# Optimization experiments

Measured on AMD Instinct MI355X. Metric: run time of the kernel, lower is better.

## Reference

```python
import jax, jax.numpy as jnp
import numpy as np

N = 128
BATCH = 4096


def _legs_transition(n):
    # HiPPO-LegS transition matrices (measure='legs' branch of transition())
    q = np.arange(n, dtype=np.float64)
    col, row = np.meshgrid(q, q)
    r = 2 * q + 1
    M = -(np.where(row >= col, r, 0) - np.diag(q))
    T = np.sqrt(np.diag(2 * q + 1))
    A = T @ M @ np.linalg.inv(T)   # lower triangular
    B = np.diag(T)                 # (n,)
    return A.astype(np.float32), B.astype(np.float32)


def setup_inputs() -> dict:
    key = jax.random.key(0)
    k1, k2, k3 = jax.random.split(key, 3)
    A, B_vec = _legs_transition(N)
    u = jax.random.normal(k1, (BATCH, N), dtype=jnp.float32)
    v = jax.random.normal(k2, (BATCH,), dtype=jnp.float32)
    # per-example step sizes, realistic small dt
    delta = 0.001 + 0.01 * jax.random.uniform(k3, (BATCH,), dtype=jnp.float32)
    return {"u": u, "v": v, "delta": delta, "A": jnp.asarray(A), "B_vec": jnp.asarray(B_vec)}


def reference(u, v, delta, A, B_vec):
    """Bilinear (Tustin) update, alpha=0.5:
       x = (I - dt/2 A)^{-1} [ (I + dt/2 A) u + dt B v ]
    Matches ManualAdaptiveTransition.bilinear with tensor delta.
    """
    n = A.shape[0]
    dt2 = 0.5 * delta                                   # (B,)
    # forward_mult: (I + dt/2 A) u  == u + dt/2 * (A u)
    x = u + dt2[:, None] * jnp.einsum('ij,bj->bi', A, u)
    # add dt * B * v
    x = x + (delta * v)[:, None] * B_vec
    # inverse_mult: batched lower-triangular solve (I - dt/2 A) y = x
    mat = jnp.eye(n, dtype=u.dtype) - dt2[:, None, None] * A   # (B, n, n)
    solve = jax.vmap(lambda m, b: jax.scipy.linalg.solve_triangular(m, b, lower=True))
    x = solve(mat, x)
    return x
```

## Files before the change

### kernel.cpp

```cpp
#include <hip/hip_runtime.h>


#define HN 128

__global__ __launch_bounds__(64) void hippo_bilinear_kernel(
    const float* __restrict__ u,
    const float* __restrict__ v,
    const float* __restrict__ delta,
    const float* __restrict__ Bv,
    float* __restrict__ out)
{
    const int b = blockIdx.x * blockDim.x + threadIdx.x;

    const float dlt = delta[b];
    const float dt2 = 0.5f * dlt;
    const float dv  = dlt * v[b];

    const float* ub = u   + (size_t)b * HN;
    float*       yb = out + (size_t)b * HN;

    float P = 0.0f;
    float S = 0.0f;

    #pragma unroll
    for (int i0 = 0; i0 < HN; i0 += 4) {
        const float4 u4 = *(const float4*)(ub + i0);
        const float4 b4 = *(const float4*)(Bv + i0);
        const float uu[4] = {u4.x, u4.y, u4.z, u4.w};
        const float vv[4] = {b4.x, b4.y, b4.z, b4.w};
        float yy[4];

        #pragma unroll
        for (int k = 0; k < 4; ++k) {
            const float vi  = vv[k];
            const float ui  = uu[k];
            const float ip1 = (float)(i0 + k + 1);

            float au = -vi * P - ip1 * ui;
            float x  = fmaf(dt2, au, ui);
            x = fmaf(dv, vi, x);

            const float d = fmaf(dt2, ip1, 1.0f);
            float r = __builtin_amdgcn_rcpf(d);
            r = r * fmaf(-d, r, 2.0f);

            const float w = dt2 * vi;
            const float y = fmaf(-w, S, x) * r;
            yy[k] = y;

            P = fmaf(vi, ui, P);
            S = fmaf(vi, y, S);
        }

        float4 y4;
        y4.x = yy[0]; y4.y = yy[1]; y4.z = yy[2]; y4.w = yy[3];
        *(float4*)(yb + i0) = y4;
    }
}

extern "C" void kernel_launch(void* const* d_in, const int* in_sizes, int n_in,
                              void* d_out, int out_size, void* d_ws, size_t ws_size,
                              hipStream_t stream) {
    const float* u     = (const float*)d_in[0];
    const float* v     = (const float*)d_in[1];
    const float* delta = (const float*)d_in[2];
    const float* Bv    = (const float*)d_in[4];
    float* out = (float*)d_out;

    const int batch = in_sizes[1];
    hippo_bilinear_kernel<<<dim3(batch / 64), dim3(64), 0, stream>>>(
        u, v, delta, Bv, out);
}
```

Measured before the change: 10.52 us.

## Parallelize triangular solve across a wavefront via affine prefix scans

Replaces the one-thread-per-row sequential recurrence with one 64-lane wavefront per batch row, each lane handling two elements. The dot-product prefix P and the solve recurrence S are computed with shuffle-based inclusive scans, the latter as a scan over affine maps. This removes the long serial dependency chain and gives coalesced float2 loads and stores instead of strided per-thread row accesses. In exchange it adds shuffle overhead and changes the floating-point summation order.

```diff
diff --git a/kernel.cpp b/kernel.cpp
--- a/kernel.cpp
+++ b/kernel.cpp
@@ -3,59 +3,83 @@
 
 #define HN 128
 
-__global__ __launch_bounds__(64) void hippo_bilinear_kernel(
+__global__ __launch_bounds__(256) void hippo_bilinear_wave_kernel(
     const float* __restrict__ u,
     const float* __restrict__ v,
     const float* __restrict__ delta,
     const float* __restrict__ Bv,
     float* __restrict__ out)
 {
-    const int b = blockIdx.x * blockDim.x + threadIdx.x;
+    const int lane = threadIdx.x & 63;
+    const int row  = blockIdx.x * (blockDim.x >> 6) + (threadIdx.x >> 6);
 
-    const float dlt = delta[b];
+    const float dlt = delta[row];
     const float dt2 = 0.5f * dlt;
-    const float dv  = dlt * v[b];
+    const float dv  = dlt * v[row];
 
-    const float* ub = u   + (size_t)b * HN;
-    float*       yb = out + (size_t)b * HN;
+    const float2 u2 = ((const float2*)(u + (size_t)row * HN))[lane];
+    const float2 b2 = ((const float2*)Bv)[lane];
 
-    float P = 0.0f;
-    float S = 0.0f;
+    const float u0 = u2.x, u1 = u2.y;
+    const float v0 = b2.x, v1 = b2.y;
+    const float ip1_0 = (float)(2 * lane + 1);
+    const float ip1_1 = (float)(2 * lane + 2);
+
+    const float p0 = v0 * u0;
+    const float p1 = v1 * u1;
+    const float ps = p0 + p1;
+    float run = ps;
+    #pragma unroll
+    for (int d = 1; d < 64; d <<= 1) {
+        const float t = __shfl_up(run, d, 64);
+        if (lane >= d) run += t;
+    }
+    const float Pexcl = run - ps;
+    const float P0 = Pexcl;
+    const float P1 = Pexcl + p0;
+
+    float x0 = fmaf(dt2, fmaf(-ip1_0, u0, -v0 * P0), u0);
+    x0 = fmaf(dv, v0, x0);
+    float x1 = fmaf(dt2, fmaf(-ip1_1, u1, -v1 * P1), u1);
+    x1 = fmaf(dv, v1, x1);
+
+    const float den0 = fmaf(dt2, ip1_0, 1.0f);
+    const float den1 = fmaf(dt2, ip1_1, 1.0f);
+    float r0 = __builtin_amdgcn_rcpf(den0);
+    r0 = r0 * fmaf(-den0, r0, 2.0f);
+    float r1 = __builtin_amdgcn_rcpf(den1);
+    r1 = r1 * fmaf(-den1, r1, 2.0f);
+
+    const float w0 = dt2 * v0;
+    const float w1 = dt2 * v1;
+    const float c0 = v0 * r0;
+    const float c1 = v1 * r1;
+    const float a0 = fmaf(-w0, c0, 1.0f);
+    const float b0 = c0 * x0;
+    const float a1 = fmaf(-w1, c1, 1.0f);
+    const float b1 = c1 * x1;
+
+    float Ai = a1 * a0;
+    float Bi = fmaf(a1, b0, b1);
 
     #pragma unroll
-    for (int i0 = 0; i0 < HN; i0 += 4) {
-        const float4 u4 = *(const float4*)(ub + i0);
-        const float4 b4 = *(const float4*)(Bv + i0);
-        const float uu[4] = {u4.x, u4.y, u4.z, u4.w};
-        const float vv[4] = {b4.x, b4.y, b4.z, b4.w};
-        float yy[4];
+    for (int d = 1; d < 64; d <<= 1) {
+        const float tA = __shfl_up(Ai, d, 64);
+        const float tB = __shfl_up(Bi, d, 64);
+        if (lane >= d) {
+            Bi = fmaf(Ai, tB, Bi);
+            Ai = Ai * tA;
+        }
+    }
+    const float Bprev = __shfl_up(Bi, 1, 64);
+    const float Sin = (lane == 0) ? 0.0f : Bprev;
 
-        #pragma unroll
-        for (int k = 0; k < 4; ++k) {
-            const float vi  = vv[k];
-            const float ui  = uu[k];
-            const float ip1 = (float)(i0 + k + 1);
+    const float y0 = fmaf(-w0, Sin, x0) * r0;
+    const float S1 = fmaf(v0, y0, Sin);
+    const float y1 = fmaf(-w1, S1, x1) * r1;
 
-            float au = -vi * P - ip1 * ui;
-            float x  = fmaf(dt2, au, ui);
-            x = fmaf(dv, vi, x);
-
-            const float d = fmaf(dt2, ip1, 1.0f);
-            float r = __builtin_amdgcn_rcpf(d);
-            r = r * fmaf(-d, r, 2.0f);
-
-            const float w = dt2 * vi;
-            const float y = fmaf(-w, S, x) * r;
-            yy[k] = y;
-
-            P = fmaf(vi, ui, P);
-            S = fmaf(vi, y, S);
-        }
-
-        float4 y4;
-        y4.x = yy[0]; y4.y = yy[1]; y4.z = yy[2]; y4.w = yy[3];
-        *(float4*)(yb + i0) = y4;
-    }
+    float2 y2; y2.x = y0; y2.y = y1;
+    ((float2*)(out + (size_t)row * HN))[lane] = y2;
 }
 
 extern "C" void kernel_launch(void* const* d_in, const int* in_sizes, int n_in,
@@ -68,6 +92,7 @@
     float* out = (float*)d_out;
 
     const int batch = in_sizes[1];
-    hippo_bilinear_kernel<<<dim3(batch / 64), dim3(64), 0, stream>>>(
+    const int rows_per_block = 4;
+    hippo_bilinear_wave_kernel<<<dim3(batch / rows_per_block), dim3(256), 0, stream>>>(
         u, v, delta, Bv, out);
 }
```

After: 9.701 us. 1.08x faster.
